# Kernel optimization log

Hardware: AMD Instinct MI355X
Metric: run time of the kernel (lower is better)

The kernel has to match this reference:

```python
import jax, jax.numpy as jnp
import numpy as np

EPS = 1e-12  # matches torch F.normalize default eps
WEIGHT = jnp.array([1.0, 1.0, 1.0], dtype=jnp.float32)  # per-channel loss weights


def _l2norm(x, axis):
    # torch F.normalize: x / max(||x||_2, eps)
    n = jnp.sqrt(jnp.sum(x * x, axis=axis, keepdims=True))
    return x / jnp.maximum(n, EPS)


def setup_inputs() -> dict:
    key = jax.random.key(0)
    k1, k2 = jax.random.split(key)
    shape = (16, 3, 512, 512)  # [B, C, H, W]
    return {
        "x": jax.random.normal(k1, shape, dtype=jnp.float32),
        "ref": jax.random.normal(k2, shape, dtype=jnp.float32),
    }


def reference(x, ref):
    # trace(rownorm(A) @ rownorm(B)^T) == sum(rownorm(A) * rownorm(B));
    # trace(colnorm(A)^T @ colnorm(B)) == sum(colnorm(A) * colnorm(B)).
    B, C, H, W = x.shape
    # per (batch, channel) traces, vectorized over all dims
    a = jnp.sum(_l2norm(x, -1) * _l2norm(ref, -1), axis=(-2, -1)) / H  # [B, C]
    b = jnp.sum(_l2norm(x, -2) * _l2norm(ref, -2), axis=(-2, -1)) / W  # [B, C]
    a = -jnp.sum(a * WEIGHT) / B
    b = -jnp.sum(b * WEIGHT) / B
    return a + b
```

## Files before the change

kernel.cpp:

```cpp
#include <hip/hip_runtime.h>

#define B_N 16
#define C_N 3
#define H_N 512
#define W_N 512
#define PLANES (B_N * C_N)
#define ROWS_PER_BLOCK 32
#define CHUNKS (H_N / ROWS_PER_BLOCK)
#define SCALE (-1.0f / 8192.0f)
#define EPS_F 1e-12f

__global__ __launch_bounds__(256) void spl_main_kernel(
    const float* __restrict__ x, const float* __restrict__ r,
    float* __restrict__ out, float* __restrict__ colws) {
    const int p     = blockIdx.x / CHUNKS;
    const int chunk = blockIdx.x % CHUNKS;
    const int wave  = threadIdx.x >> 6;
    const int lane  = threadIdx.x & 63;

    const float* xp = x + (size_t)p * (H_N * W_N);
    const float* rp = r + (size_t)p * (H_N * W_N);

    float cxx[8] = {0, 0, 0, 0, 0, 0, 0, 0};
    float crr[8] = {0, 0, 0, 0, 0, 0, 0, 0};
    float cxr[8] = {0, 0, 0, 0, 0, 0, 0, 0};
    float rowacc = 0.0f;

    const int r0 = chunk * ROWS_PER_BLOCK;
    for (int j = 0; j < ROWS_PER_BLOCK / 4; ++j) {
        const int row = r0 + wave + 4 * j;
        const float4* xr4 = (const float4*)(xp + (size_t)row * W_N);
        const float4* rr4 = (const float4*)(rp + (size_t)row * W_N);
        const float4 xa = xr4[lane];
        const float4 xb = xr4[lane + 64];
        const float4 ra = rr4[lane];
        const float4 rb = rr4[lane + 64];

        cxx[0] += xa.x * xa.x; cxx[1] += xa.y * xa.y; cxx[2] += xa.z * xa.z; cxx[3] += xa.w * xa.w;
        cxx[4] += xb.x * xb.x; cxx[5] += xb.y * xb.y; cxx[6] += xb.z * xb.z; cxx[7] += xb.w * xb.w;
        crr[0] += ra.x * ra.x; crr[1] += ra.y * ra.y; crr[2] += ra.z * ra.z; crr[3] += ra.w * ra.w;
        crr[4] += rb.x * rb.x; crr[5] += rb.y * rb.y; crr[6] += rb.z * rb.z; crr[7] += rb.w * rb.w;
        cxr[0] += xa.x * ra.x; cxr[1] += xa.y * ra.y; cxr[2] += xa.z * ra.z; cxr[3] += xa.w * ra.w;
        cxr[4] += xb.x * rb.x; cxr[5] += xb.y * rb.y; cxr[6] += xb.z * rb.z; cxr[7] += xb.w * rb.w;

        float sxx = xa.x * xa.x + xa.y * xa.y + xa.z * xa.z + xa.w * xa.w
                  + xb.x * xb.x + xb.y * xb.y + xb.z * xb.z + xb.w * xb.w;
        float srr = ra.x * ra.x + ra.y * ra.y + ra.z * ra.z + ra.w * ra.w
                  + rb.x * rb.x + rb.y * rb.y + rb.z * rb.z + rb.w * rb.w;
        float sxr = xa.x * ra.x + xa.y * ra.y + xa.z * ra.z + xa.w * ra.w
                  + xb.x * rb.x + xb.y * rb.y + xb.z * rb.z + xb.w * rb.w;
        #pragma unroll
        for (int m = 32; m > 0; m >>= 1) {
            sxx += __shfl_down(sxx, m, 64);
            srr += __shfl_down(srr, m, 64);
            sxr += __shfl_down(sxr, m, 64);
        }
        if (lane == 0) {
            const float nx = fmaxf(sqrtf(sxx), EPS_F);
            const float nr = fmaxf(sqrtf(srr), EPS_F);
            rowacc += sxr / (nx * nr);
        }
    }

    __shared__ float smem[4][W_N * 3];
    #pragma unroll
    for (int k = 0; k < 4; ++k) {
        const int c0 = 4 * lane + k;
        const int c1 = c0 + 256;
        smem[wave][c0 * 3 + 0] = cxx[k];
        smem[wave][c0 * 3 + 1] = crr[k];
        smem[wave][c0 * 3 + 2] = cxr[k];
        smem[wave][c1 * 3 + 0] = cxx[4 + k];
        smem[wave][c1 * 3 + 1] = crr[4 + k];
        smem[wave][c1 * 3 + 2] = cxr[4 + k];
    }
    __shared__ float rowsums[4];
    if (lane == 0) rowsums[wave] = rowacc;
    __syncthreads();

    for (int e = threadIdx.x; e < W_N * 3; e += 256) {
        const float v = smem[0][e] + smem[1][e] + smem[2][e] + smem[3][e];
        atomicAdd(&colws[(size_t)p * (W_N * 3) + e], v);
    }
    if (threadIdx.x == 0) {
        const float t = rowsums[0] + rowsums[1] + rowsums[2] + rowsums[3];
        atomicAdd(out, SCALE * t);
    }
}

__global__ __launch_bounds__(256) void spl_cols_kernel(
    const float* __restrict__ colws, float* __restrict__ out) {
    const int idx = blockIdx.x * 256 + threadIdx.x;
    float term = 0.0f;
    if (idx < PLANES * W_N) {
        const float sxx = colws[idx * 3 + 0];
        const float srr = colws[idx * 3 + 1];
        const float sxr = colws[idx * 3 + 2];
        const float nx = fmaxf(sqrtf(sxx), EPS_F);
        const float nr = fmaxf(sqrtf(srr), EPS_F);
        term = sxr / (nx * nr);
    }
    #pragma unroll
    for (int m = 32; m > 0; m >>= 1) term += __shfl_down(term, m, 64);
    __shared__ float ws[4];
    const int lane = threadIdx.x & 63, wave = threadIdx.x >> 6;
    if (lane == 0) ws[wave] = term;
    __syncthreads();
    if (threadIdx.x == 0)
        atomicAdd(out, SCALE * (ws[0] + ws[1] + ws[2] + ws[3]));
}

extern "C" void kernel_launch(void* const* d_in, const int* in_sizes, int n_in,
                              void* d_out, int out_size, void* d_ws, size_t ws_size,
                              hipStream_t stream) {
    const float* x   = (const float*)d_in[0];
    const float* ref = (const float*)d_in[1];
    float* out   = (float*)d_out;
    float* colws = (float*)d_ws;

    hipMemsetAsync(colws, 0, (size_t)PLANES * W_N * 3 * sizeof(float), stream);
    hipMemsetAsync(out, 0, sizeof(float), stream);
    spl_main_kernel<<<PLANES * CHUNKS, 256, 0, stream>>>(x, ref, out, colws);
    spl_cols_kernel<<<(PLANES * W_N) / 256, 256, 0, stream>>>(colws, out);
}
```

Measured before the change: 126.3 us.

## Replace atomic column accumulation with per-block partials and deterministic reduction kernels

```diff
diff --git a/kernel.cpp b/kernel.cpp
--- a/kernel.cpp
+++ b/kernel.cpp
@@ -7,12 +7,14 @@
 #define PLANES (B_N * C_N)
 #define ROWS_PER_BLOCK 32
 #define CHUNKS (H_N / ROWS_PER_BLOCK)
+#define NBLK (PLANES * CHUNKS)
+#define STATS3 (W_N * 3)
 #define SCALE (-1.0f / 8192.0f)
 #define EPS_F 1e-12f
 
 __global__ __launch_bounds__(256) void spl_main_kernel(
     const float* __restrict__ x, const float* __restrict__ r,
-    float* __restrict__ out, float* __restrict__ colws) {
+    float* __restrict__ colpart, float* __restrict__ rowpart) {
     const int p     = blockIdx.x / CHUNKS;
     const int chunk = blockIdx.x % CHUNKS;
     const int wave  = threadIdx.x >> 6;
@@ -43,12 +45,15 @@
         cxr[0] += xa.x * ra.x; cxr[1] += xa.y * ra.y; cxr[2] += xa.z * ra.z; cxr[3] += xa.w * ra.w;
         cxr[4] += xb.x * rb.x; cxr[5] += xb.y * rb.y; cxr[6] += xb.z * rb.z; cxr[7] += xb.w * rb.w;
 
-        float sxx = xa.x * xa.x + xa.y * xa.y + xa.z * xa.z + xa.w * xa.w
-                  + xb.x * xb.x + xb.y * xb.y + xb.z * xb.z + xb.w * xb.w;
-        float srr = ra.x * ra.x + ra.y * ra.y + ra.z * ra.z + ra.w * ra.w
-                  + rb.x * rb.x + rb.y * rb.y + rb.z * rb.z + rb.w * rb.w;
-        float sxr = xa.x * ra.x + xa.y * ra.y + xa.z * ra.z + xa.w * ra.w
-                  + xb.x * rb.x + xb.y * rb.y + xb.z * rb.z + xb.w * rb.w;
+        float sxx = cxx[0] + cxx[1] + cxx[2] + cxx[3] + cxx[4] + cxx[5] + cxx[6] + cxx[7];
+        float srr = crr[0] + crr[1] + crr[2] + crr[3] + crr[4] + crr[5] + crr[6] + crr[7];
+        float sxr = cxr[0] + cxr[1] + cxr[2] + cxr[3] + cxr[4] + cxr[5] + cxr[6] + cxr[7];
+        sxx = xa.x * xa.x + xa.y * xa.y + xa.z * xa.z + xa.w * xa.w
+            + xb.x * xb.x + xb.y * xb.y + xb.z * xb.z + xb.w * xb.w;
+        srr = ra.x * ra.x + ra.y * ra.y + ra.z * ra.z + ra.w * ra.w
+            + rb.x * rb.x + rb.y * rb.y + rb.z * rb.z + rb.w * rb.w;
+        sxr = xa.x * ra.x + xa.y * ra.y + xa.z * ra.z + xa.w * ra.w
+            + xb.x * rb.x + xb.y * rb.y + xb.z * rb.z + xb.w * rb.w;
         #pragma unroll
         for (int m = 32; m > 0; m >>= 1) {
             sxx += __shfl_down(sxx, m, 64);
@@ -62,7 +67,7 @@
         }
     }
 
-    __shared__ float smem[4][W_N * 3];
+    __shared__ float smem[4][STATS3];
     #pragma unroll
     for (int k = 0; k < 4; ++k) {
         const int c0 = 4 * lane + k;
@@ -78,36 +83,57 @@
     if (lane == 0) rowsums[wave] = rowacc;
     __syncthreads();
 
-    for (int e = threadIdx.x; e < W_N * 3; e += 256) {
-        const float v = smem[0][e] + smem[1][e] + smem[2][e] + smem[3][e];
-        atomicAdd(&colws[(size_t)p * (W_N * 3) + e], v);
+    float* cp = colpart + (size_t)blockIdx.x * STATS3;
+    #pragma unroll
+    for (int k = 0; k < 6; ++k) {
+        const int e = threadIdx.x + 256 * k;
+        cp[e] = smem[0][e] + smem[1][e] + smem[2][e] + smem[3][e];
     }
-    if (threadIdx.x == 0) {
-        const float t = rowsums[0] + rowsums[1] + rowsums[2] + rowsums[3];
-        atomicAdd(out, SCALE * t);
-    }
+    if (threadIdx.x == 0)
+        rowpart[blockIdx.x] = rowsums[0] + rowsums[1] + rowsums[2] + rowsums[3];
 }
 
-__global__ __launch_bounds__(256) void spl_cols_kernel(
-    const float* __restrict__ colws, float* __restrict__ out) {
-    const int idx = blockIdx.x * 256 + threadIdx.x;
+__global__ __launch_bounds__(256) void spl_reduce_kernel(
+    const float* __restrict__ colpart, const float* __restrict__ rowpart,
+    float* __restrict__ planesum) {
+    const int p = blockIdx.x;
+    float acc[6] = {0, 0, 0, 0, 0, 0};
+    const float* base = colpart + (size_t)p * CHUNKS * STATS3;
+    for (int c = 0; c < CHUNKS; ++c) {
+        const float* bc = base + c * STATS3;
+        #pragma unroll
+        for (int k = 0; k < 6; ++k) acc[k] += bc[threadIdx.x + 256 * k];
+    }
+    __shared__ float sums[STATS3];
+    #pragma unroll
+    for (int k = 0; k < 6; ++k) sums[threadIdx.x + 256 * k] = acc[k];
+    __syncthreads();
+
     float term = 0.0f;
-    if (idx < PLANES * W_N) {
-        const float sxx = colws[idx * 3 + 0];
-        const float srr = colws[idx * 3 + 1];
-        const float sxr = colws[idx * 3 + 2];
-        const float nx = fmaxf(sqrtf(sxx), EPS_F);
-        const float nr = fmaxf(sqrtf(srr), EPS_F);
-        term = sxr / (nx * nr);
+    #pragma unroll
+    for (int k = 0; k < 2; ++k) {
+        const int col = threadIdx.x + 256 * k;
+        const float sxx = sums[col * 3 + 0];
+        const float srr = sums[col * 3 + 1];
+        const float sxr = sums[col * 3 + 2];
+        term += sxr / (fmaxf(sqrtf(sxx), EPS_F) * fmaxf(sqrtf(srr), EPS_F));
     }
+    if (threadIdx.x < CHUNKS) term += rowpart[p * CHUNKS + threadIdx.x];
+
     #pragma unroll
     for (int m = 32; m > 0; m >>= 1) term += __shfl_down(term, m, 64);
     __shared__ float ws[4];
-    const int lane = threadIdx.x & 63, wave = threadIdx.x >> 6;
-    if (lane == 0) ws[wave] = term;
+    if ((threadIdx.x & 63) == 0) ws[threadIdx.x >> 6] = term;
     __syncthreads();
-    if (threadIdx.x == 0)
-        atomicAdd(out, SCALE * (ws[0] + ws[1] + ws[2] + ws[3]));
+    if (threadIdx.x == 0) planesum[p] = ws[0] + ws[1] + ws[2] + ws[3];
+}
+
+__global__ void spl_final_kernel(const float* __restrict__ planesum,
+                                 float* __restrict__ out) {
+    float v = (threadIdx.x < PLANES) ? planesum[threadIdx.x] : 0.0f;
+    #pragma unroll
+    for (int m = 32; m > 0; m >>= 1) v += __shfl_down(v, m, 64);
+    if (threadIdx.x == 0) out[0] = SCALE * v;
 }
 
 extern "C" void kernel_launch(void* const* d_in, const int* in_sizes, int n_in,
@@ -115,11 +141,13 @@
                               hipStream_t stream) {
     const float* x   = (const float*)d_in[0];
     const float* ref = (const float*)d_in[1];
-    float* out   = (float*)d_out;
-    float* colws = (float*)d_ws;
+    float* out = (float*)d_out;
 
-    hipMemsetAsync(colws, 0, (size_t)PLANES * W_N * 3 * sizeof(float), stream);
-    hipMemsetAsync(out, 0, sizeof(float), stream);
-    spl_main_kernel<<<PLANES * CHUNKS, 256, 0, stream>>>(x, ref, out, colws);
-    spl_cols_kernel<<<(PLANES * W_N) / 256, 256, 0, stream>>>(colws, out);
+    float* colpart  = (float*)d_ws;
+    float* rowpart  = colpart + (size_t)NBLK * STATS3;
+    float* planesum = rowpart + NBLK;
+
+    spl_main_kernel<<<NBLK, 256, 0, stream>>>(x, ref, colpart, rowpart);
+    spl_reduce_kernel<<<PLANES, 256, 0, stream>>>(colpart, rowpart, planesum);
+    spl_final_kernel<<<1, 64, 0, stream>>>(planesum, out);
 }
```

Result: faster. 119.9 us (-5.1%).
